# Kernel optimization log

Hardware: AMD Instinct MI355X
Metric: run time of the kernel (lower is better)

Reference implementation:

```python
import jax, jax.numpy as jnp
import numpy as np
from jax import lax
from jax.scipy.linalg import expm

B, T, H, NCLS = 256, 784, 512, 10


def setup_inputs() -> dict:
    key = jax.random.key(0)
    ks = jax.random.split(key, 6)
    inputs = jax.random.normal(ks[0], (B, T), dtype=jnp.float32)
    # faithful to Model: fixed permutation from RandomState(92916)
    permutation = jnp.asarray(np.random.RandomState(92916).permutation(T), dtype=jnp.int64)
    W_skew = jax.random.normal(ks[1], (H, H), dtype=jnp.float32) * 0.05  # free param for skew-symmetric A
    W_in = jax.random.normal(ks[2], (H, 1), dtype=jnp.float32)            # Linear(1, H, bias=False)
    b_mod = jax.random.uniform(ks[3], (H,), dtype=jnp.float32, minval=-0.01, maxval=0.01)  # modrelu bias
    W_lin = jax.random.normal(ks[4], (NCLS, H), dtype=jnp.float32) * 0.05
    b_lin = jax.random.normal(ks[5], (NCLS,), dtype=jnp.float32) * 0.05
    return {"inputs": inputs, "permutation": permutation, "W_skew": W_skew,
            "W_in": W_in, "b_mod": b_mod, "W_lin": W_lin, "b_lin": b_lin}


def reference(inputs, permutation, W_skew, W_in, b_mod, W_lin, b_lin):
    # permuted-pixel input sequence: [B, T]
    x = inputs[:, permutation]
    # expm parametrization of the orthogonal recurrent kernel:
    # A = triu(W,1) - triu(W,1)^T (skew-symmetric), Borth = expm(A) is orthogonal
    Au = jnp.triu(W_skew, 1)
    Borth = expm(Au - Au.T)  # [H, H]
    # precompute all input projections: Linear(1,H) on each scalar pixel -> [T, B, H]
    proj = x.T[:, :, None] * W_in[:, 0][None, None, :]

    def step(h, u):
        pre = u + h @ Borth                                  # [B, H]
        h_new = jnp.sign(pre) * jax.nn.relu(jnp.abs(pre) + b_mod)  # modrelu
        return h_new, None

    h0 = jnp.zeros((inputs.shape[0], W_in.shape[0]), dtype=inputs.dtype)
    hT, _ = lax.scan(step, h0, proj)
    return hT @ W_lin.T + b_lin  # [B, 10]
```

## Files before the change

### kernel.cpp

```cpp
#include <hip/hip_runtime.h>

#define TSTEPS 784
#define BATCH  256
#define HDIM   512
#define NCLS   10
#define NGRP   16
#define WGPG   8

typedef __bf16 bf16x8 __attribute__((ext_vector_type(8)));
typedef float  f32x4  __attribute__((ext_vector_type(4)));
typedef unsigned uint4v __attribute__((ext_vector_type(4)));

static __device__ __forceinline__ unsigned short f2bf(float f) {
  unsigned u = __builtin_bit_cast(unsigned, f);
  u += 0x7fffu + ((u >> 16) & 1u);
  return (unsigned short)(u >> 16);
}
static __device__ __forceinline__ float bf2f(unsigned s) {
  unsigned u = s << 16;
  return __builtin_bit_cast(float, u);
}

__global__ __launch_bounds__(256) void gather_xp(const float* __restrict__ in,
                                                 const int* __restrict__ perm,
                                                 float* __restrict__ xp) {
  int t = blockIdx.x;
  int b = threadIdx.x;
  int p = perm[t];
  p = (p < 0) ? 0 : (p >= TSTEPS ? TSTEPS - 1 : p);
  xp[t * BATCH + b] = in[b * TSTEPS + p];
}

__global__ __launch_bounds__(256) void build_X(const float* __restrict__ W,
                                               float* __restrict__ X) {
  int idx = blockIdx.x * 256 + threadIdx.x;
  int i = idx >> 9, j = idx & 511;
  float v = 0.f;
  if (j > i) v = W[i * HDIM + j];
  else if (i > j) v = -W[j * HDIM + i];
  X[idx] = v * 0.03125f;
}

__global__ __launch_bounds__(256) void axpyI(float* __restrict__ P,
                                             const float* __restrict__ X, float coef) {
  int idx = blockIdx.x * 256 + threadIdx.x;
  int i = idx >> 9, j = idx & 511;
  P[idx] = coef * X[idx] + ((i == j) ? 1.f : 0.f);
}

__global__ __launch_bounds__(256) void gemm512(float* __restrict__ C,
                                               const float* __restrict__ A,
                                               const float* __restrict__ B,
                                               float alpha, int addI) {
  __shared__ float As[16][68];
  __shared__ float Bs[16][68];
  const int tx = threadIdx.x, ty = threadIdx.y;
  const int tid = ty * 16 + tx;
  const int ib = blockIdx.y, jb = blockIdx.x;
  const int ra = tid >> 2, ca = (tid & 3) << 2;
  const int rb = tid >> 4, cb = (tid & 15) << 2;
  float acc[4][4] = {};
  for (int kt = 0; kt < HDIM / 16; ++kt) {
    f32x4 av = *(const f32x4*)(A + (ib * 64 + ra) * HDIM + kt * 16 + ca);
    f32x4 bv = *(const f32x4*)(B + (kt * 16 + rb) * HDIM + jb * 64 + cb);
    __syncthreads();
    As[ca + 0][ra] = av[0];
    As[ca + 1][ra] = av[1];
    As[ca + 2][ra] = av[2];
    As[ca + 3][ra] = av[3];
    *(f32x4*)&Bs[rb][cb] = bv;
    __syncthreads();
#pragma unroll
    for (int kk = 0; kk < 16; ++kk) {
      f32x4 a4 = *(const f32x4*)&As[kk][ty << 2];
      f32x4 b4 = *(const f32x4*)&Bs[kk][tx << 2];
#pragma unroll
      for (int u = 0; u < 4; ++u)
#pragma unroll
        for (int v = 0; v < 4; ++v) acc[u][v] = fmaf(a4[u], b4[v], acc[u][v]);
    }
  }
#pragma unroll
  for (int u = 0; u < 4; ++u)
#pragma unroll
    for (int v = 0; v < 4; ++v) {
      int r = ib * 64 + (ty << 2) + u, c = jb * 64 + (tx << 2) + v;
      float val = alpha * acc[u][v];
      if (addI && r == c) val += 1.f;
      C[r * HDIM + c] = val;
    }
}

__global__ __launch_bounds__(256, 1) void rnn_main(
    const float* __restrict__ xp, const float* __restrict__ Borth,
    const float* __restrict__ W_in, const float* __restrict__ b_mod,
    const float* __restrict__ W_lin, const float* __restrict__ b_lin,
    unsigned* __restrict__ h0p, unsigned* __restrict__ h1p,
    unsigned* __restrict__ flags, float* __restrict__ out) {
  __shared__ unsigned tileA[16 * HDIM];

  const int wg = blockIdx.x;
  const int gb = wg & 15;
  const int cg = wg >> 4;
  const int tid = threadIdx.x;
  const int wave = tid >> 6;
  const int lane = tid & 63;
  const int quad = lane >> 4;
  const int l16 = lane & 15;
  const int colg = (cg << 6) + (wave << 4) + l16;

  bf16x8 Bhi[16], Blo[16];
#pragma unroll
  for (int ki = 0; ki < 16; ++ki) {
#pragma unroll
    for (int j = 0; j < 8; ++j) {
      int k = (ki << 5) + (quad << 3) + j;
      float v = Borth[k * HDIM + colg];
      unsigned short hb = f2bf(v);
      unsigned short lb = f2bf(v - bf2f(hb));
      Bhi[ki][j] = __builtin_bit_cast(__bf16, hb);
      Blo[ki][j] = __builtin_bit_cast(__bf16, lb);
    }
  }
  const float win = W_in[colg];
  const float bm = b_mod[colg];

  unsigned* const gbase0 = h0p + (gb << 13);
  unsigned* const gbase1 = h1p + (gb << 13);
  unsigned* const myflag = flags + ((gb << 3) + cg) * 32;
  unsigned* const gflags = flags + (gb << 3) * 32;
  const unsigned swz = (unsigned)((l16 & 7) << 2);

  for (int t = 0; t < TSTEPS; ++t) {
    const unsigned* __restrict__ cur = (t & 1) ? gbase1 : gbase0;
    unsigned* __restrict__ nxt = (t & 1) ? gbase0 : gbase1;

    unsigned long long q[16];
    const unsigned long long* curq = (const unsigned long long*)cur;
#pragma unroll
    for (int i = 0; i < 16; ++i)
      q[i] = __hip_atomic_load(curq + tid + (i << 8), __ATOMIC_RELAXED,
                               __HIP_MEMORY_SCOPE_AGENT);
#pragma unroll
    for (int i = 0; i < 16; ++i) {
      unsigned phys = ((unsigned)i << 9) | (((unsigned)(tid << 1)) ^ ((i & 7) << 2));
      *(unsigned long long*)(tileA + phys) = q[i];
    }
    __syncthreads();

    f32x4 a_hh = {0.f, 0.f, 0.f, 0.f};
    f32x4 a_lh = {0.f, 0.f, 0.f, 0.f};
    f32x4 a_hl = {0.f, 0.f, 0.f, 0.f};
#pragma unroll
    for (int ki = 0; ki < 16; ++ki) {
      int c0 = (ki << 5) + (quad << 3);
      const unsigned* lp0 = tileA + (l16 << 9) + ((unsigned)c0 ^ swz);
      const unsigned* lp1 = tileA + (l16 << 9) + ((unsigned)(c0 + 4) ^ swz);
      uint4v d0 = *(const uint4v*)lp0;
      uint4v d1 = *(const uint4v*)lp1;
      unsigned d[8] = {d0[0], d0[1], d0[2], d0[3], d1[0], d1[1], d1[2], d1[3]};
      uint4v vh, vl;
#pragma unroll
      for (int p = 0; p < 4; ++p) {
        vh[p] = __builtin_amdgcn_perm(d[2 * p + 1], d[2 * p], 0x07060302u);
        vl[p] = __builtin_amdgcn_perm(d[2 * p + 1], d[2 * p], 0x05040100u);
      }
      bf16x8 ah = __builtin_bit_cast(bf16x8, vh);
      bf16x8 al = __builtin_bit_cast(bf16x8, vl);
      a_hh = __builtin_amdgcn_mfma_f32_16x16x32_bf16(ah, Bhi[ki], a_hh, 0, 0, 0);
      a_lh = __builtin_amdgcn_mfma_f32_16x16x32_bf16(al, Bhi[ki], a_lh, 0, 0, 0);
      a_hl = __builtin_amdgcn_mfma_f32_16x16x32_bf16(ah, Blo[ki], a_hl, 0, 0, 0);
    }

    const f32x4 xps = *(const f32x4*)(xp + t * BATCH + (gb << 4) + (quad << 2));
#pragma unroll
    for (int r = 0; r < 4; ++r) {
      float pre = a_hh[r] + a_lh[r] + a_hl[r] + xps[r] * win;
      float mm = fmaxf(fabsf(pre) + bm, 0.f);
      float hv = (pre > 0.f) ? mm : ((pre < 0.f) ? -mm : 0.f);
      int idx = (((quad << 2) + r) << 9) + colg;
      unsigned short hbv = f2bf(hv);
      unsigned short lbv = f2bf(hv - bf2f(hbv));
      unsigned pk = ((unsigned)hbv << 16) | (unsigned)lbv;
      __hip_atomic_store(nxt + idx, pk, __ATOMIC_RELAXED, __HIP_MEMORY_SCOPE_AGENT);
    }

    asm volatile("s_waitcnt vmcnt(0)" ::: "memory");
    __syncthreads();
    if (tid == 0)
      __hip_atomic_store(myflag, (unsigned)(t + 1), __ATOMIC_RELAXED,
                         __HIP_MEMORY_SCOPE_AGENT);
    const unsigned target = (unsigned)(t + 1);
    int spin = 0;
    for (;;) {
      unsigned fl = __hip_atomic_load(gflags + (lane & 7) * 32, __ATOMIC_RELAXED,
                                      __HIP_MEMORY_SCOPE_AGENT);
      if (__ballot(fl >= target) == ~0ull) break;
      __builtin_amdgcn_s_sleep(1);
      if (++spin > (1 << 22)) break;
    }
  }

  if (cg == 0) {
    int row = tid >> 4;
    int cls = tid & 15;
    if (cls < NCLS) {
      const unsigned* hf = gbase0 + (row << 9);
      float s = b_lin[cls];
      const float* wl = W_lin + cls * HDIM;
      for (int k = 0; k < HDIM; ++k) {
        unsigned p = __hip_atomic_load(hf + k, __ATOMIC_RELAXED, __HIP_MEMORY_SCOPE_AGENT);
        float hvv = bf2f(p >> 16) + bf2f(p & 0xffffu);
        s = fmaf(hvv, wl[k], s);
      }
      out[((gb << 4) + row) * NCLS + cls] = s;
    }
  }
}

extern "C" void kernel_launch(void* const* d_in, const int* in_sizes, int n_in,
                              void* d_out, int out_size, void* d_ws, size_t ws_size,
                              hipStream_t stream) {
  const float* inputs = (const float*)d_in[0];
  const int* perm = (const int*)d_in[1];
  const float* W_skew = (const float*)d_in[2];
  const float* W_in = (const float*)d_in[3];
  const float* b_mod = (const float*)d_in[4];
  const float* W_lin = (const float*)d_in[5];
  const float* b_lin = (const float*)d_in[6];
  float* out = (float*)d_out;

  char* ws = (char*)d_ws;
  unsigned* flags = (unsigned*)ws;
  unsigned* h0p = (unsigned*)(ws + 32768);
  unsigned* h1p = h0p + BATCH * HDIM;
  float* xp = (float*)(h1p + BATCH * HDIM);
  float* X = xp + TSTEPS * BATCH;
  float* P = X + HDIM * HDIM;
  float* Q = P + HDIM * HDIM;

  hipMemsetAsync(flags, 0, 32768, stream);
  hipMemsetAsync(h0p, 0, (size_t)BATCH * HDIM * sizeof(unsigned), stream);

  gather_xp<<<TSTEPS, 256, 0, stream>>>(inputs, perm, xp);
  build_X<<<(HDIM * HDIM) / 256, 256, 0, stream>>>(W_skew, X);

  axpyI<<<(HDIM * HDIM) / 256, 256, 0, stream>>>(P, X, 1.f / 6.f);
  float* a = P;
  float* b = Q;
  for (int k = 5; k >= 1; --k) {
    gemm512<<<dim3(8, 8), dim3(16, 16), 0, stream>>>(b, X, a, 1.f / (float)k, 1);
    float* tmp = a; a = b; b = tmp;
  }
  for (int i = 0; i < 5; ++i) {
    gemm512<<<dim3(8, 8), dim3(16, 16), 0, stream>>>(b, a, a, 1.f, 0);
    float* tmp = a; a = b; b = tmp;
  }

  rnn_main<<<NGRP * WGPG, 256, 0, stream>>>(xp, a, W_in, b_mod, W_lin, b_lin,
                                            h0p, h1p, flags, out);
  (void)in_sizes; (void)n_in; (void)out_size; (void)ws_size;
}
```

Before: 2.556 ms.

## Replace flag barrier with step-tagged hidden-state words polled directly

```diff
diff --git a/kernel.cpp b/kernel.cpp
--- a/kernel.cpp
+++ b/kernel.cpp
@@ -10,6 +10,7 @@
 typedef __bf16 bf16x8 __attribute__((ext_vector_type(8)));
 typedef float  f32x4  __attribute__((ext_vector_type(4)));
 typedef unsigned uint4v __attribute__((ext_vector_type(4)));
+typedef unsigned long long u64;
 
 static __device__ __forceinline__ unsigned short f2bf(float f) {
   unsigned u = __builtin_bit_cast(unsigned, f);
@@ -19,6 +20,12 @@
 static __device__ __forceinline__ float bf2f(unsigned s) {
   unsigned u = s << 16;
   return __builtin_bit_cast(float, u);
+}
+static __device__ __forceinline__ u64 ald(const u64* p) {
+  return __hip_atomic_load(p, __ATOMIC_RELAXED, __HIP_MEMORY_SCOPE_AGENT);
+}
+static __device__ __forceinline__ void ast(u64* p, u64 v) {
+  __hip_atomic_store(p, v, __ATOMIC_RELAXED, __HIP_MEMORY_SCOPE_AGENT);
 }
 
 __global__ __launch_bounds__(256) void gather_xp(const float* __restrict__ in,
@@ -95,8 +102,7 @@
     const float* __restrict__ xp, const float* __restrict__ Borth,
     const float* __restrict__ W_in, const float* __restrict__ b_mod,
     const float* __restrict__ W_lin, const float* __restrict__ b_lin,
-    unsigned* __restrict__ h0p, unsigned* __restrict__ h1p,
-    unsigned* __restrict__ flags, float* __restrict__ out) {
+    u64* __restrict__ h0, u64* __restrict__ h1, float* __restrict__ out) {
   __shared__ unsigned tileA[16 * HDIM];
 
   const int wg = blockIdx.x;
@@ -125,29 +131,44 @@
   const float win = W_in[colg];
   const float bm = b_mod[colg];
 
-  unsigned* const gbase0 = h0p + (gb << 13);
-  unsigned* const gbase1 = h1p + (gb << 13);
-  unsigned* const myflag = flags + ((gb << 3) + cg) * 32;
-  unsigned* const gflags = flags + (gb << 3) * 32;
-  const unsigned swz = (unsigned)((l16 & 7) << 2);
+  u64* const g0 = h0 + (gb << 13);
+  u64* const g1 = h1 + (gb << 13);
+  const int e0 = tid << 1;
 
   for (int t = 0; t < TSTEPS; ++t) {
-    const unsigned* __restrict__ cur = (t & 1) ? gbase1 : gbase0;
-    unsigned* __restrict__ nxt = (t & 1) ? gbase0 : gbase1;
-
-    unsigned long long q[16];
-    const unsigned long long* curq = (const unsigned long long*)cur;
-#pragma unroll
-    for (int i = 0; i < 16; ++i)
-      q[i] = __hip_atomic_load(curq + tid + (i << 8), __ATOMIC_RELAXED,
-                               __HIP_MEMORY_SCOPE_AGENT);
+    const u64* __restrict__ cur = (t & 1) ? g1 : g0;
+    u64* __restrict__ nxt = (t & 1) ? g0 : g1;
+    const unsigned tg = (unsigned)t;
+
+    u64 qa[16], qb[16];
 #pragma unroll
     for (int i = 0; i < 16; ++i) {
-      unsigned phys = ((unsigned)i << 9) | (((unsigned)(tid << 1)) ^ ((i & 7) << 2));
-      *(unsigned long long*)(tileA + phys) = q[i];
-    }
-    __syncthreads();
-
+      qa[i] = ald(cur + (i << 9) + e0);
+      qb[i] = ald(cur + (i << 9) + e0 + 1);
+    }
+    int spin = 0;
+    for (;;) {
+      bool ok = true;
+#pragma unroll
+      for (int i = 0; i < 16; ++i)
+        ok = ok && ((unsigned)(qa[i] >> 32) == tg) && ((unsigned)(qb[i] >> 32) == tg);
+      if (__ballot(ok) == ~0ull) break;
+      if (++spin > (1 << 20)) break;
+      __builtin_amdgcn_s_sleep(1);
+#pragma unroll
+      for (int i = 0; i < 16; ++i) {
+        if ((unsigned)(qa[i] >> 32) != tg) qa[i] = ald(cur + (i << 9) + e0);
+        if ((unsigned)(qb[i] >> 32) != tg) qb[i] = ald(cur + (i << 9) + e0 + 1);
+      }
+    }
+#pragma unroll
+    for (int i = 0; i < 16; ++i) {
+      unsigned phys = ((unsigned)i << 9) | (((unsigned)e0) ^ ((i & 7) << 2));
+      *(u64*)(tileA + phys) = (u64)(unsigned)qa[i] | ((u64)(unsigned)qb[i] << 32);
+    }
+    __syncthreads();
+
+    const unsigned swz = (unsigned)((l16 & 7) << 2);
     f32x4 a_hh = {0.f, 0.f, 0.f, 0.f};
     f32x4 a_lh = {0.f, 0.f, 0.f, 0.f};
     f32x4 a_hl = {0.f, 0.f, 0.f, 0.f};
@@ -173,45 +194,37 @@
     }
 
     const f32x4 xps = *(const f32x4*)(xp + t * BATCH + (gb << 4) + (quad << 2));
+    const u64 tagw = ((u64)(unsigned)(t + 1)) << 32;
 #pragma unroll
     for (int r = 0; r < 4; ++r) {
       float pre = a_hh[r] + a_lh[r] + a_hl[r] + xps[r] * win;
       float mm = fmaxf(fabsf(pre) + bm, 0.f);
       float hv = (pre > 0.f) ? mm : ((pre < 0.f) ? -mm : 0.f);
-      int idx = (((quad << 2) + r) << 9) + colg;
+      int row = (quad << 2) + r;
       unsigned short hbv = f2bf(hv);
       unsigned short lbv = f2bf(hv - bf2f(hbv));
-      unsigned pk = ((unsigned)hbv << 16) | (unsigned)lbv;
-      __hip_atomic_store(nxt + idx, pk, __ATOMIC_RELAXED, __HIP_MEMORY_SCOPE_AGENT);
-    }
-
-    asm volatile("s_waitcnt vmcnt(0)" ::: "memory");
-    __syncthreads();
-    if (tid == 0)
-      __hip_atomic_store(myflag, (unsigned)(t + 1), __ATOMIC_RELAXED,
-                         __HIP_MEMORY_SCOPE_AGENT);
-    const unsigned target = (unsigned)(t + 1);
-    int spin = 0;
-    for (;;) {
-      unsigned fl = __hip_atomic_load(gflags + (lane & 7) * 32, __ATOMIC_RELAXED,
-                                      __HIP_MEMORY_SCOPE_AGENT);
-      if (__ballot(fl >= target) == ~0ull) break;
-      __builtin_amdgcn_s_sleep(1);
-      if (++spin > (1 << 22)) break;
-    }
+      u64 val = (u64)(((unsigned)hbv << 16) | (unsigned)lbv) | tagw;
+      ast(nxt + (row << 9) + colg, val);
+    }
+    __syncthreads();
   }
 
   if (cg == 0) {
     int row = tid >> 4;
     int cls = tid & 15;
     if (cls < NCLS) {
-      const unsigned* hf = gbase0 + (row << 9);
+      const u64* hf = g0 + (row << 9);
       float s = b_lin[cls];
       const float* wl = W_lin + cls * HDIM;
       for (int k = 0; k < HDIM; ++k) {
-        unsigned p = __hip_atomic_load(hf + k, __ATOMIC_RELAXED, __HIP_MEMORY_SCOPE_AGENT);
-        float hvv = bf2f(p >> 16) + bf2f(p & 0xffffu);
-        s = fmaf(hvv, wl[k], s);
+        u64 qv = ald(hf + k);
+        int sp = 0;
+        while ((unsigned)(qv >> 32) != (unsigned)TSTEPS) {
+          qv = ald(hf + k);
+          if (++sp > (1 << 20)) break;
+        }
+        unsigned p = (unsigned)qv;
+        s = fmaf(bf2f(p >> 16) + bf2f(p & 0xffffu), wl[k], s);
       }
       out[((gb << 4) + row) * NCLS + cls] = s;
     }
@@ -231,16 +244,12 @@
   float* out = (float*)d_out;
 
   char* ws = (char*)d_ws;
-  unsigned* flags = (unsigned*)ws;
-  unsigned* h0p = (unsigned*)(ws + 32768);
-  unsigned* h1p = h0p + BATCH * HDIM;
-  float* xp = (float*)(h1p + BATCH * HDIM);
-  float* X = xp + TSTEPS * BATCH;
-  float* P = X + HDIM * HDIM;
-  float* Q = P + HDIM * HDIM;
-
-  hipMemsetAsync(flags, 0, 32768, stream);
-  hipMemsetAsync(h0p, 0, (size_t)BATCH * HDIM * sizeof(unsigned), stream);
+  float* X = (float*)ws;
+  float* P = (float*)(ws + (1 << 20));
+  float* Q = (float*)(ws + (2 << 20));
+  float* xp = (float*)(ws + (3 << 20));
+  u64* h0 = (u64*)ws;
+  u64* h1 = (u64*)(ws + (2 << 20));
 
   gather_xp<<<TSTEPS, 256, 0, stream>>>(inputs, perm, xp);
   build_X<<<(HDIM * HDIM) / 256, 256, 0, stream>>>(W_skew, X);
@@ -257,7 +266,9 @@
     float* tmp = a; a = b; b = tmp;
   }
 
-  rnn_main<<<NGRP * WGPG, 256, 0, stream>>>(xp, a, W_in, b_mod, W_lin, b_lin,
-                                            h0p, h1p, flags, out);
+  hipMemsetAsync(h0, 0, (size_t)NGRP * 8192 * sizeof(u64), stream);
+  hipMemsetAsync(h1, 0, (size_t)NGRP * 8192 * sizeof(u64), stream);
+
+  rnn_main<<<NGRP * WGPG, 256, 0, stream>>>(xp, a, W_in, b_mod, W_lin, b_lin, h0, h1, out);
   (void)in_sizes; (void)n_in; (void)out_size; (void)ws_size;
 }
```

Result: slower. 2.900 ms (+13.4%).
